# Kernel tuning notes

Measured on AMD Instinct MI355X. Metric: run time of the kernel, lower is better.

The kernel has to match this reference:

```python
import jax, jax.numpy as jnp
import numpy as np

N = 50000
E = 1600000
VOCAB = 1000
EMB = 128
HID = 128
OUT = 128


def setup_inputs() -> dict:
    key = jax.random.key(0)
    ks = jax.random.split(key, 8)
    labels = jax.random.randint(ks[0], (N,), 0, VOCAB)
    edge_index = jax.random.randint(ks[1], (2, E), 0, N)
    weight = jax.random.uniform(ks[2], (E,), dtype=jnp.float32)
    emb_table = jax.random.normal(ks[3], (VOCAB, EMB), dtype=jnp.float32) * 0.02
    W1 = jax.random.normal(ks[4], (EMB, HID), dtype=jnp.float32) * (1.0 / np.sqrt(EMB))
    b1 = jnp.zeros((HID,), dtype=jnp.float32)
    W2 = jax.random.normal(ks[5], (HID, OUT), dtype=jnp.float32) * (1.0 / np.sqrt(HID))
    b2 = jnp.zeros((OUT,), dtype=jnp.float32)
    return {"labels": labels, "edge_index": edge_index, "weight": weight,
            "emb_table": emb_table, "W1": W1, "b1": b1, "W2": W2, "b2": b2}


def _gcn_conv(x, src, dst, ew, W, b, n_nodes):
    # PyG GCNConv: linear transform, then symmetric-normalized weighted aggregation.
    x = x @ W  # [N, F_out]
    deg = jax.ops.segment_sum(ew, dst, num_segments=n_nodes)  # weighted in-degree (incl. self loops)
    dinv = jnp.where(deg > 0, jax.lax.rsqrt(deg), 0.0)
    norm = dinv[src] * ew * dinv[dst]  # [E_tot]
    msg = x[src] * norm[:, None]  # gather + scale
    out = jax.ops.segment_sum(msg, dst, num_segments=n_nodes)  # scatter-add
    return out + b


def reference(labels, edge_index, weight, emb_table, W1, b1, W2, b2):
    n_nodes = emb_table.shape[0] if False else labels.shape[0]
    # add self loops with weight 1.0 (GCNConv default add_self_loops=True)
    loop = jnp.arange(n_nodes, dtype=edge_index.dtype)
    src = jnp.concatenate([edge_index[0], loop])
    dst = jnp.concatenate([edge_index[1], loop])
    ew = jnp.concatenate([weight.astype(jnp.float32), jnp.ones((n_nodes,), jnp.float32)])

    x = emb_table[labels]  # embedding lookup [N, EMB]
    x = _gcn_conv(x, src, dst, ew, W1, b1, n_nodes)
    x = jax.nn.relu(x)
    x = _gcn_conv(x, src, dst, ew, W2, b2, n_nodes)
    return x
```

## Files before the change

kernel.cpp:

```cpp
#include <hip/hip_runtime.h>
#include <hip/hip_fp16.h>


#define CHUNKS 256

__global__ __launch_bounds__(256) void hist_kernel(const int* __restrict__ dst,
                                                   int* __restrict__ hist,
                                                   int e, int chunk, int nb) {
  __shared__ unsigned lh[1024];
  int b = blockIdx.x, t = threadIdx.x;
  int start = b * chunk, end = min(e, start + chunk);
  for (int i = t; i < nb; i += 256) lh[i] = 0;
  __syncthreads();
  for (int i = start + t; i < end; i += 256) atomicAdd(&lh[dst[i] >> 6], 1u);
  __syncthreads();
  for (int k = t; k < nb; k += 256) hist[(size_t)k * CHUNKS + b] = (int)lh[k];
}

__global__ __launch_bounds__(256) void colscan_kernel(const int* __restrict__ hist,
                                                      int* __restrict__ off,
                                                      int* __restrict__ tot,
                                                      int nb, int bact) {
  int k = (blockIdx.x * 256 + threadIdx.x) >> 6;
  int lane = threadIdx.x & 63;
  if (k >= nb) return;
  int carry = 0;
  for (int r = 0; r < CHUNKS / 64; ++r) {
    int b = r * 64 + lane;
    int h = (b < bact) ? hist[(size_t)k * CHUNKS + b] : 0;
    int x = h;
#pragma unroll
    for (int d = 1; d < 64; d <<= 1) {
      int tt = __shfl_up(x, d, 64);
      if (lane >= d) x += tt;
    }
    if (b < bact) off[(size_t)k * CHUNKS + b] = carry + x - h;
    carry += __shfl(x, 63, 64);
  }
  if (lane == 0) tot[k] = carry;
}

__global__ __launch_bounds__(1024) void ebase_kernel(const int* __restrict__ tot,
                                                     int* __restrict__ ebase, int nb) {
  __shared__ int wsum[16];
  int t = threadIdx.x, lane = t & 63, wv = t >> 6;
  int v = (t < nb) ? tot[t] : 0;
  int x = v;
#pragma unroll
  for (int d = 1; d < 64; d <<= 1) {
    int tt = __shfl_up(x, d, 64);
    if (lane >= d) x += tt;
  }
  if (lane == 63) wsum[wv] = x;
  __syncthreads();
  int o = 0;
#pragma unroll
  for (int w = 0; w < 16; ++w) o += (w < wv) ? wsum[w] : 0;
  int excl = x - v + o;
  if (t < nb) ebase[t] = excl;
  if (t == nb - 1) ebase[nb] = excl + v;
}

__global__ __launch_bounds__(256) void scatter_kernel(
    const int* __restrict__ src, const int* __restrict__ dst,
    const float* __restrict__ w, const int* __restrict__ labels,
    const int* __restrict__ off, const int* __restrict__ ebase,
    int2* __restrict__ brec, int e, int chunk) {
  __shared__ unsigned bincnt[1024];
  int b = blockIdx.x, t = threadIdx.x;
  int start = b * chunk, end = min(e, start + chunk);
  for (int i = t; i < 1024; i += 256) bincnt[i] = 0;
  __syncthreads();
  for (int bs0 = start; bs0 < end; bs0 += 1792) {
    int bend = min(end, bs0 + 1792);
    int s[7], d[7], lb[7], ps[7];
    float wv[7];
#pragma unroll
    for (int u = 0; u < 7; ++u) {
      int i = bs0 + u * 256 + t;
      bool ok = i < bend;
      s[u] = ok ? src[i] : 0;
      d[u] = ok ? dst[i] : 0;
      wv[u] = ok ? w[i] : 0.f;
    }
#pragma unroll
    for (int u = 0; u < 7; ++u) lb[u] = labels[s[u]];
#pragma unroll
    for (int u = 0; u < 7; ++u) {
      int k = d[u] >> 6;
      ps[u] = ebase[k] + off[(size_t)k * CHUNKS + b];
    }
#pragma unroll
    for (int u = 0; u < 7; ++u) {
      int i = bs0 + u * 256 + t;
      if (i < bend) {
        int k = d[u] >> 6;
        unsigned lr = atomicAdd(&bincnt[k], 1u);
        unsigned rx = (unsigned)s[u] | ((unsigned)(d[u] & 63) << 16) |
                      ((unsigned)lb[u] << 22);
        brec[ps[u] + (int)lr] = make_int2((int)rx, __float_as_int(wv[u]));
      }
    }
  }
}

__global__ __launch_bounds__(256) void bsort_kernel(const int2* __restrict__ brec,
                                                    const int* __restrict__ ebase,
                                                    int2* __restrict__ csr,
                                                    int* __restrict__ rs,
                                                    float* __restrict__ dinv, int n) {
  __shared__ unsigned h64[64];
  __shared__ unsigned cur[64];
  __shared__ float rsum[64];
  int k = blockIdx.x, t = threadIdx.x;
  int e0 = ebase[k], e1 = ebase[k + 1];
  if (t < 64) { h64[t] = 0; rsum[t] = 0.f; }
  __syncthreads();
  for (int i = e0 + t; i < e1; i += 256) {
    int2 r = brec[i];
    unsigned dl = ((unsigned)r.x >> 16) & 63u;
    atomicAdd(&h64[dl], 1u);
    atomicAdd(&rsum[dl], __int_as_float(r.y));
  }
  __syncthreads();
  if (t < 64) {
    int hv = (int)h64[t];
    int x = hv;
#pragma unroll
    for (int d = 1; d < 64; d <<= 1) {
      int tt = __shfl_up(x, d, 64);
      if (t >= d) x += tt;
    }
    int ex = x - hv;
    cur[t] = (unsigned)(e0 + ex);
    int v = k * 64 + t;
    if (v <= n) rs[v] = e0 + ex;
    if (v < n) dinv[v] = rsqrtf(1.0f + rsum[t]);
  }
  __syncthreads();
  for (int i = e0 + t; i < e1; i += 256) {
    int2 r = brec[i];
    unsigned rx = (unsigned)r.x;
    int dl = (int)((rx >> 16) & 63u);
    int pos = (int)atomicAdd(&cur[dl], 1u);
    csr[pos] = make_int2((int)((rx & 0xffffu) | ((rx >> 22) << 16)), r.y);
  }
}

__global__ void temb_kernel(const float* __restrict__ emb, const float* __restrict__ W1,
                            __half* __restrict__ temb) {
  int r = blockIdx.x, j = threadIdx.x;
  __shared__ float xs[128];
  xs[j] = emb[r * 128 + j];
  __syncthreads();
  float acc = 0.f;
#pragma unroll 8
  for (int k = 0; k < 128; ++k) acc = fmaf(xs[k], W1[k * 128 + j], acc);
  temb[r * 128 + j] = __float2half_rn(acc);
}

__device__ __forceinline__ void unpack4(float2 raw, float2& a, float2& b) {
  union { float f; __half2 h; } u0, u1;
  u0.f = raw.x;
  u1.f = raw.y;
  a = __half22float2(u0.h);
  b = __half22float2(u1.h);
}

__global__ __launch_bounds__(256) void agg1_kernel(
    const int* __restrict__ rs, const int2* __restrict__ csr,
    const float* __restrict__ dinv, const int* __restrict__ labels,
    const __half* __restrict__ temb, const float* __restrict__ b1,
    __half* __restrict__ out1, int n) {
  int wid = (blockIdx.x * blockDim.x + threadIdx.x) >> 6;
  int lane = threadIdx.x & 63;
  if (wid >= n) return;
  int half = lane >> 5, fl = lane & 31;
  float di = dinv[wid];
  float acc0, acc1, acc2, acc3;
  {
    int selfrow = labels[wid];
    float2 raw = ((const float2*)(temb + (size_t)selfrow * 128))[fl];
    float2 a, b;
    unpack4(raw, a, b);
    float ss = half ? 0.f : di;
    acc0 = a.x * ss; acc1 = a.y * ss; acc2 = b.x * ss; acc3 = b.y * ss;
  }
  int r1v = rs[wid + 1];
  for (int base = rs[wid]; base < r1v; base += 64) {
    int s = 0;
    float v = 0.f;
    if (base + lane < r1v) {
      int2 c = csr[base + lane];
      s = c.x;
      v = __int_as_float(c.y) * dinv[c.x & 0xffff];
    }
    int nb = min(64, r1v - base);
    int j = 0;
    for (; j + 16 <= nb; j += 16) {
#pragma unroll
      for (int u = 0; u < 8; ++u) {
        int jj = j + 2 * u + half;
        int sj = __shfl(s, jj, 64);
        float vj = __shfl(v, jj, 64);
        float2 raw = ((const float2*)(temb + (size_t)(sj >> 16) * 128))[fl];
        float2 a, b;
        unpack4(raw, a, b);
        acc0 = fmaf(a.x, vj, acc0); acc1 = fmaf(a.y, vj, acc1);
        acc2 = fmaf(b.x, vj, acc2); acc3 = fmaf(b.y, vj, acc3);
      }
    }
    for (; j + 2 <= nb; j += 2) {
      int jj = j + half;
      int sj = __shfl(s, jj, 64);
      float vj = __shfl(v, jj, 64);
      float2 raw = ((const float2*)(temb + (size_t)(sj >> 16) * 128))[fl];
      float2 a, b;
      unpack4(raw, a, b);
      acc0 = fmaf(a.x, vj, acc0); acc1 = fmaf(a.y, vj, acc1);
      acc2 = fmaf(b.x, vj, acc2); acc3 = fmaf(b.y, vj, acc3);
    }
    if (j < nb) {
      int sj = __shfl(s, j, 64);
      float vj0 = __shfl(v, j, 64);
      float vj = half ? 0.f : vj0;
      float2 raw = ((const float2*)(temb + (size_t)(sj >> 16) * 128))[fl];
      float2 a, b;
      unpack4(raw, a, b);
      acc0 = fmaf(a.x, vj, acc0); acc1 = fmaf(a.y, vj, acc1);
      acc2 = fmaf(b.x, vj, acc2); acc3 = fmaf(b.y, vj, acc3);
    }
  }
  acc0 += __shfl_xor(acc0, 32, 64);
  acc1 += __shfl_xor(acc1, 32, 64);
  acc2 += __shfl_xor(acc2, 32, 64);
  acc3 += __shfl_xor(acc3, 32, 64);
  if (half == 0) {
    float4 b4 = ((const float4*)b1)[fl];
    acc0 = fmaxf(fmaf(acc0, di, b4.x), 0.f);
    acc1 = fmaxf(fmaf(acc1, di, b4.y), 0.f);
    acc2 = fmaxf(fmaf(acc2, di, b4.z), 0.f);
    acc3 = fmaxf(fmaf(acc3, di, b4.w), 0.f);
    union { float2 f2; __half2 h2[2]; } o;
    o.h2[0] = __float22half2_rn(make_float2(acc0, acc1));
    o.h2[1] = __float22half2_rn(make_float2(acc2, acc3));
    ((float2*)(out1 + (size_t)wid * 128))[fl] = o.f2;
  }
}

__global__ __launch_bounds__(256) void agg2_kernel(
    const int* __restrict__ rs, const int2* __restrict__ csr,
    const float* __restrict__ dinv, const __half* __restrict__ h,
    float* __restrict__ out, int n) {
  int wid = (blockIdx.x * blockDim.x + threadIdx.x) >> 6;
  int lane = threadIdx.x & 63;
  if (wid >= n) return;
  int half = lane >> 5, fl = lane & 31;
  float di = dinv[wid];
  float acc0, acc1, acc2, acc3;
  {
    float2 raw = ((const float2*)(h + (size_t)wid * 128))[fl];
    float2 a, b;
    unpack4(raw, a, b);
    float ss = half ? 0.f : di;
    acc0 = a.x * ss; acc1 = a.y * ss; acc2 = b.x * ss; acc3 = b.y * ss;
  }
  int r1v = rs[wid + 1];
  for (int base = rs[wid]; base < r1v; base += 64) {
    int s = 0;
    float v = 0.f;
    if (base + lane < r1v) {
      int2 c = csr[base + lane];
      s = c.x;
      v = __int_as_float(c.y) * dinv[c.x & 0xffff];
    }
    int nb = min(64, r1v - base);
    int j = 0;
    for (; j + 16 <= nb; j += 16) {
#pragma unroll
      for (int u = 0; u < 8; ++u) {
        int jj = j + 2 * u + half;
        int sj = __shfl(s, jj, 64);
        float vj = __shfl(v, jj, 64);
        float2 raw = ((const float2*)(h + (size_t)(sj & 0xffff) * 128))[fl];
        float2 a, b;
        unpack4(raw, a, b);
        acc0 = fmaf(a.x, vj, acc0); acc1 = fmaf(a.y, vj, acc1);
        acc2 = fmaf(b.x, vj, acc2); acc3 = fmaf(b.y, vj, acc3);
      }
    }
    for (; j + 2 <= nb; j += 2) {
      int jj = j + half;
      int sj = __shfl(s, jj, 64);
      float vj = __shfl(v, jj, 64);
      float2 raw = ((const float2*)(h + (size_t)(sj & 0xffff) * 128))[fl];
      float2 a, b;
      unpack4(raw, a, b);
      acc0 = fmaf(a.x, vj, acc0); acc1 = fmaf(a.y, vj, acc1);
      acc2 = fmaf(b.x, vj, acc2); acc3 = fmaf(b.y, vj, acc3);
    }
    if (j < nb) {
      int sj = __shfl(s, j, 64);
      float vj0 = __shfl(v, j, 64);
      float vj = half ? 0.f : vj0;
      float2 raw = ((const float2*)(h + (size_t)(sj & 0xffff) * 128))[fl];
      float2 a, b;
      unpack4(raw, a, b);
      acc0 = fmaf(a.x, vj, acc0); acc1 = fmaf(a.y, vj, acc1);
      acc2 = fmaf(b.x, vj, acc2); acc3 = fmaf(b.y, vj, acc3);
    }
  }
  acc0 += __shfl_xor(acc0, 32, 64);
  acc1 += __shfl_xor(acc1, 32, 64);
  acc2 += __shfl_xor(acc2, 32, 64);
  acc3 += __shfl_xor(acc3, 32, 64);
  if (half == 0) {
    ((float4*)(out + (size_t)wid * 128))[fl] =
        make_float4(acc0 * di, acc1 * di, acc2 * di, acc3 * di);
  }
}

__global__ __launch_bounds__(256) void gemm_bias_kernel(float* __restrict__ y,
                                                        const float* __restrict__ W,
                                                        const float* __restrict__ bias,
                                                        int n) {
  __shared__ float xs[32][128];
  int tid = threadIdx.x;
  int tc = tid & 31;
  int tr = tid >> 5;
  int rb = blockIdx.x * 32;
  {
    const float4* xg = (const float4*)(y + (size_t)rb * 128);
    float4* xls = (float4*)&xs[0][0];
#pragma unroll
    for (int i = 0; i < 4; ++i) {
      int idx = tid + i * 256;
      int row = rb + (idx >> 5);
      float4 val = (row < n) ? xg[idx] : make_float4(0.f, 0.f, 0.f, 0.f);
      xls[idx] = val;
    }
  }
  __syncthreads();
  int j0 = tc * 4;
  float4 b4 = *(const float4*)(bias + j0);
  float acc[4][4];
#pragma unroll
  for (int r = 0; r < 4; ++r) {
    acc[r][0] = b4.x; acc[r][1] = b4.y; acc[r][2] = b4.z; acc[r][3] = b4.w;
  }
#pragma unroll 4
  for (int k = 0; k < 128; ++k) {
    float4 w4 = *(const float4*)(W + k * 128 + j0);
#pragma unroll
    for (int r = 0; r < 4; ++r) {
      float xv = xs[tr * 4 + r][k];
      acc[r][0] = fmaf(xv, w4.x, acc[r][0]);
      acc[r][1] = fmaf(xv, w4.y, acc[r][1]);
      acc[r][2] = fmaf(xv, w4.z, acc[r][2]);
      acc[r][3] = fmaf(xv, w4.w, acc[r][3]);
    }
  }
#pragma unroll
  for (int r = 0; r < 4; ++r) {
    int row = rb + tr * 4 + r;
    if (row < n)
      *(float4*)(y + (size_t)row * 128 + j0) =
          make_float4(acc[r][0], acc[r][1], acc[r][2], acc[r][3]);
  }
}

extern "C" void kernel_launch(void* const* d_in, const int* in_sizes, int n_in,
                              void* d_out, int out_size, void* d_ws, size_t ws_size,
                              hipStream_t stream) {
  const int* labels = (const int*)d_in[0];
  const int* edge_index = (const int*)d_in[1];
  const float* weight = (const float*)d_in[2];
  const float* emb = (const float*)d_in[3];
  const float* W1 = (const float*)d_in[4];
  const float* b1 = (const float*)d_in[5];
  const float* W2 = (const float*)d_in[6];
  const float* b2 = (const float*)d_in[7];

  int n = in_sizes[0];
  int e = in_sizes[1] / 2;
  int vocab = in_sizes[3] / 128;
  const int* srcp = edge_index;
  const int* dstp = edge_index + e;

  int nb = (n + 63) >> 6;
  int chunk = (e + CHUNKS - 1) / CHUNKS;
  int bact = (e + chunk - 1) / chunk;

  float* ws = (float*)d_ws;
  size_t o = 0;
  auto alloc_f = [&](size_t c) { float* p = ws + o; o += (c + 255) & ~(size_t)255; return p; };
  int*    hist  = (int*)alloc_f((size_t)nb * CHUNKS);
  int*    off   = (int*)alloc_f((size_t)nb * CHUNKS);
  int*    tot   = (int*)alloc_f(nb);
  int*    ebase = (int*)alloc_f(nb + 1);
  int2*   brec  = (int2*)alloc_f((size_t)e * 2);
  int*    rs    = (int*)alloc_f(n + 1);
  int2*   csr   = (int2*)alloc_f((size_t)e * 2);
  float*  dinv  = alloc_f(n);
  __half* temb  = (__half*)alloc_f((size_t)vocab * 64);
  __half* out1  = (__half*)alloc_f((size_t)n * 64);
  (void)ws_size;

  dim3 b256(256);
  int gagg = (int)(((size_t)n * 64 + 255) / 256);

  hist_kernel<<<bact, b256, 0, stream>>>(dstp, hist, e, chunk, nb);
  colscan_kernel<<<(nb * 64 + 255) / 256, b256, 0, stream>>>(hist, off, tot, nb, bact);
  ebase_kernel<<<1, 1024, 0, stream>>>(tot, ebase, nb);
  scatter_kernel<<<bact, b256, 0, stream>>>(srcp, dstp, weight, labels, off, ebase,
                                            brec, e, chunk);
  bsort_kernel<<<nb, b256, 0, stream>>>(brec, ebase, csr, rs, dinv, n);
  temb_kernel<<<vocab, 128, 0, stream>>>(emb, W1, temb);
  agg1_kernel<<<gagg, b256, 0, stream>>>(rs, csr, dinv, labels, temb, b1, out1, n);
  agg2_kernel<<<gagg, b256, 0, stream>>>(rs, csr, dinv, out1, (float*)d_out, n);
  gemm_bias_kernel<<<(n + 31) / 32, b256, 0, stream>>>((float*)d_out, W2, b2, n);
}
```

Baseline: 200.5 us.

## Column-chunk layer-2 features and aggregate in four L2-resident passes

```diff
diff --git a/kernel.cpp b/kernel.cpp
--- a/kernel.cpp
+++ b/kernel.cpp
@@ -171,7 +171,7 @@
     const int* __restrict__ rs, const int2* __restrict__ csr,
     const float* __restrict__ dinv, const int* __restrict__ labels,
     const __half* __restrict__ temb, const float* __restrict__ b1,
-    __half* __restrict__ out1, int n) {
+    __half* __restrict__ out1c, int n) {
   int wid = (blockIdx.x * blockDim.x + threadIdx.x) >> 6;
   int lane = threadIdx.x & 63;
   if (wid >= n) return;
@@ -244,78 +244,58 @@
     union { float2 f2; __half2 h2[2]; } o;
     o.h2[0] = __float22half2_rn(make_float2(acc0, acc1));
     o.h2[1] = __float22half2_rn(make_float2(acc2, acc3));
-    ((float2*)(out1 + (size_t)wid * 128))[fl] = o.f2;
-  }
-}
-
-__global__ __launch_bounds__(256) void agg2_kernel(
+    ((float2*)(out1c + (((size_t)(fl >> 3) * n + wid) * 32)))[fl & 7] = o.f2;
+  }
+}
+
+__global__ __launch_bounds__(256) void agg2c_kernel(
     const int* __restrict__ rs, const int2* __restrict__ csr,
-    const float* __restrict__ dinv, const __half* __restrict__ h,
-    float* __restrict__ out, int n) {
+    const float* __restrict__ dinv, const __half* __restrict__ hc,
+    float* __restrict__ out, int n, int c) {
   int wid = (blockIdx.x * blockDim.x + threadIdx.x) >> 6;
   int lane = threadIdx.x & 63;
   if (wid >= n) return;
-  int half = lane >> 5, fl = lane & 31;
+  int grp = lane >> 3, fl = lane & 7;
   float di = dinv[wid];
-  float acc0, acc1, acc2, acc3;
-  {
-    float2 raw = ((const float2*)(h + (size_t)wid * 128))[fl];
+  float acc0 = 0.f, acc1 = 0.f, acc2 = 0.f, acc3 = 0.f;
+  if (grp == 0) {
+    float2 raw = ((const float2*)(hc + (size_t)wid * 32))[fl];
     float2 a, b;
     unpack4(raw, a, b);
-    float ss = half ? 0.f : di;
-    acc0 = a.x * ss; acc1 = a.y * ss; acc2 = b.x * ss; acc3 = b.y * ss;
+    acc0 = a.x * di; acc1 = a.y * di; acc2 = b.x * di; acc3 = b.y * di;
   }
   int r1v = rs[wid + 1];
   for (int base = rs[wid]; base < r1v; base += 64) {
     int s = 0;
     float v = 0.f;
     if (base + lane < r1v) {
-      int2 c = csr[base + lane];
-      s = c.x;
-      v = __int_as_float(c.y) * dinv[c.x & 0xffff];
+      int2 cc = csr[base + lane];
+      s = cc.x;
+      v = __int_as_float(cc.y) * dinv[cc.x & 0xffff];
     }
     int nb = min(64, r1v - base);
-    int j = 0;
-    for (; j + 16 <= nb; j += 16) {
-#pragma unroll
-      for (int u = 0; u < 8; ++u) {
-        int jj = j + 2 * u + half;
-        int sj = __shfl(s, jj, 64);
-        float vj = __shfl(v, jj, 64);
-        float2 raw = ((const float2*)(h + (size_t)(sj & 0xffff) * 128))[fl];
+#pragma unroll
+    for (int jstep = 0; jstep < 8; ++jstep) {
+      if (jstep * 8 < nb) {
+        int j = jstep * 8 + grp;
+        int sj = __shfl(s, j, 64);
+        float vj = __shfl(v, j, 64);
+        float2 raw = ((const float2*)(hc + (size_t)(sj & 0xffff) * 32))[fl];
         float2 a, b;
         unpack4(raw, a, b);
         acc0 = fmaf(a.x, vj, acc0); acc1 = fmaf(a.y, vj, acc1);
         acc2 = fmaf(b.x, vj, acc2); acc3 = fmaf(b.y, vj, acc3);
       }
     }
-    for (; j + 2 <= nb; j += 2) {
-      int jj = j + half;
-      int sj = __shfl(s, jj, 64);
-      float vj = __shfl(v, jj, 64);
-      float2 raw = ((const float2*)(h + (size_t)(sj & 0xffff) * 128))[fl];
-      float2 a, b;
-      unpack4(raw, a, b);
-      acc0 = fmaf(a.x, vj, acc0); acc1 = fmaf(a.y, vj, acc1);
-      acc2 = fmaf(b.x, vj, acc2); acc3 = fmaf(b.y, vj, acc3);
-    }
-    if (j < nb) {
-      int sj = __shfl(s, j, 64);
-      float vj0 = __shfl(v, j, 64);
-      float vj = half ? 0.f : vj0;
-      float2 raw = ((const float2*)(h + (size_t)(sj & 0xffff) * 128))[fl];
-      float2 a, b;
-      unpack4(raw, a, b);
-      acc0 = fmaf(a.x, vj, acc0); acc1 = fmaf(a.y, vj, acc1);
-      acc2 = fmaf(b.x, vj, acc2); acc3 = fmaf(b.y, vj, acc3);
-    }
-  }
-  acc0 += __shfl_xor(acc0, 32, 64);
-  acc1 += __shfl_xor(acc1, 32, 64);
-  acc2 += __shfl_xor(acc2, 32, 64);
-  acc3 += __shfl_xor(acc3, 32, 64);
-  if (half == 0) {
-    ((float4*)(out + (size_t)wid * 128))[fl] =
+  }
+  acc0 += __shfl_xor(acc0, 8, 64);  acc1 += __shfl_xor(acc1, 8, 64);
+  acc2 += __shfl_xor(acc2, 8, 64);  acc3 += __shfl_xor(acc3, 8, 64);
+  acc0 += __shfl_xor(acc0, 16, 64); acc1 += __shfl_xor(acc1, 16, 64);
+  acc2 += __shfl_xor(acc2, 16, 64); acc3 += __shfl_xor(acc3, 16, 64);
+  acc0 += __shfl_xor(acc0, 32, 64); acc1 += __shfl_xor(acc1, 32, 64);
+  acc2 += __shfl_xor(acc2, 32, 64); acc3 += __shfl_xor(acc3, 32, 64);
+  if (grp == 0) {
+    ((float4*)(out + (size_t)wid * 128 + 32 * c))[fl] =
         make_float4(acc0 * di, acc1 * di, acc2 * di, acc3 * di);
   }
 }
@@ -403,7 +383,7 @@
   int2*   csr   = (int2*)alloc_f((size_t)e * 2);
   float*  dinv  = alloc_f(n);
   __half* temb  = (__half*)alloc_f((size_t)vocab * 64);
-  __half* out1  = (__half*)alloc_f((size_t)n * 64);
+  __half* out1c = (__half*)alloc_f((size_t)n * 64);
   (void)ws_size;
 
   dim3 b256(256);
@@ -416,7 +396,11 @@
                                             brec, e, chunk);
   bsort_kernel<<<nb, b256, 0, stream>>>(brec, ebase, csr, rs, dinv, n);
   temb_kernel<<<vocab, 128, 0, stream>>>(emb, W1, temb);
-  agg1_kernel<<<gagg, b256, 0, stream>>>(rs, csr, dinv, labels, temb, b1, out1, n);
-  agg2_kernel<<<gagg, b256, 0, stream>>>(rs, csr, dinv, out1, (float*)d_out, n);
+  agg1_kernel<<<gagg, b256, 0, stream>>>(rs, csr, dinv, labels, temb, b1, out1c, n);
+  for (int c = 0; c < 4; ++c) {
+    agg2c_kernel<<<gagg, b256, 0, stream>>>(rs, csr, dinv,
+                                            out1c + (size_t)c * n * 32,
+                                            (float*)d_out, n, c);
+  }
   gemm_bias_kernel<<<(n + 31) / 32, b256, 0, stream>>>((float*)d_out, W2, b2, n);
 }
```

Result: slower. 259.8 us (+29.6%).

## Widen sort-phase blocks to 1024 threads, cache bin bases, stage bucket records in LDS

Applied to the files above, without the earlier changes.

```diff
diff --git a/kernel.cpp b/kernel.cpp
--- a/kernel.cpp
+++ b/kernel.cpp
@@ -3,18 +3,19 @@
 
 
 #define CHUNKS 256
-
-__global__ __launch_bounds__(256) void hist_kernel(const int* __restrict__ dst,
-                                                   int* __restrict__ hist,
-                                                   int e, int chunk, int nb) {
+#define BSTAGE 2816
+
+__global__ __launch_bounds__(1024) void hist_kernel(const int* __restrict__ dst,
+                                                    int* __restrict__ hist,
+                                                    int e, int chunk, int nb) {
   __shared__ unsigned lh[1024];
   int b = blockIdx.x, t = threadIdx.x;
+  lh[t] = 0;
+  __syncthreads();
   int start = b * chunk, end = min(e, start + chunk);
-  for (int i = t; i < nb; i += 256) lh[i] = 0;
-  __syncthreads();
-  for (int i = start + t; i < end; i += 256) atomicAdd(&lh[dst[i] >> 6], 1u);
-  __syncthreads();
-  for (int k = t; k < nb; k += 256) hist[(size_t)k * CHUNKS + b] = (int)lh[k];
+  for (int i = start + t; i < end; i += 1024) atomicAdd(&lh[dst[i] >> 6], 1u);
+  __syncthreads();
+  if (t < nb) hist[(size_t)t * CHUNKS + b] = (int)lh[t];
 }
 
 __global__ __launch_bounds__(256) void colscan_kernel(const int* __restrict__ hist,
@@ -61,45 +62,41 @@
   if (t == nb - 1) ebase[nb] = excl + v;
 }
 
-__global__ __launch_bounds__(256) void scatter_kernel(
+__global__ __launch_bounds__(1024) void scatter_kernel(
     const int* __restrict__ src, const int* __restrict__ dst,
     const float* __restrict__ w, const int* __restrict__ labels,
     const int* __restrict__ off, const int* __restrict__ ebase,
-    int2* __restrict__ brec, int e, int chunk) {
+    int2* __restrict__ brec, int e, int chunk, int nb) {
   __shared__ unsigned bincnt[1024];
+  __shared__ int gbase[1024];
   int b = blockIdx.x, t = threadIdx.x;
+  bincnt[t] = 0;
+  if (t < nb) gbase[t] = ebase[t] + off[(size_t)t * CHUNKS + b];
+  __syncthreads();
   int start = b * chunk, end = min(e, start + chunk);
-  for (int i = t; i < 1024; i += 256) bincnt[i] = 0;
-  __syncthreads();
-  for (int bs0 = start; bs0 < end; bs0 += 1792) {
-    int bend = min(end, bs0 + 1792);
-    int s[7], d[7], lb[7], ps[7];
-    float wv[7];
-#pragma unroll
-    for (int u = 0; u < 7; ++u) {
-      int i = bs0 + u * 256 + t;
-      bool ok = i < bend;
-      s[u] = ok ? src[i] : 0;
-      d[u] = ok ? dst[i] : 0;
-      wv[u] = ok ? w[i] : 0.f;
-    }
-#pragma unroll
-    for (int u = 0; u < 7; ++u) lb[u] = labels[s[u]];
-#pragma unroll
-    for (int u = 0; u < 7; ++u) {
+  int s[7], d[7], lb[7], ps[7];
+  float wv[7];
+#pragma unroll
+  for (int u = 0; u < 7; ++u) {
+    int i = start + u * 1024 + t;
+    bool ok = i < end;
+    s[u] = ok ? src[i] : 0;
+    d[u] = ok ? dst[i] : 0;
+    wv[u] = ok ? w[i] : 0.f;
+  }
+#pragma unroll
+  for (int u = 0; u < 7; ++u) lb[u] = labels[s[u]];
+#pragma unroll
+  for (int u = 0; u < 7; ++u) ps[u] = gbase[d[u] >> 6];
+#pragma unroll
+  for (int u = 0; u < 7; ++u) {
+    int i = start + u * 1024 + t;
+    if (i < end) {
       int k = d[u] >> 6;
-      ps[u] = ebase[k] + off[(size_t)k * CHUNKS + b];
-    }
-#pragma unroll
-    for (int u = 0; u < 7; ++u) {
-      int i = bs0 + u * 256 + t;
-      if (i < bend) {
-        int k = d[u] >> 6;
-        unsigned lr = atomicAdd(&bincnt[k], 1u);
-        unsigned rx = (unsigned)s[u] | ((unsigned)(d[u] & 63) << 16) |
-                      ((unsigned)lb[u] << 22);
-        brec[ps[u] + (int)lr] = make_int2((int)rx, __float_as_int(wv[u]));
-      }
+      unsigned lr = atomicAdd(&bincnt[k], 1u);
+      unsigned rx = (unsigned)s[u] | ((unsigned)(d[u] & 63) << 16) |
+                    ((unsigned)lb[u] << 22);
+      brec[ps[u] + (int)lr] = make_int2((int)rx, __float_as_int(wv[u]));
     }
   }
 }
@@ -109,15 +106,18 @@
                                                     int2* __restrict__ csr,
                                                     int* __restrict__ rs,
                                                     float* __restrict__ dinv, int n) {
+  __shared__ int2 stage[BSTAGE];
   __shared__ unsigned h64[64];
   __shared__ unsigned cur[64];
   __shared__ float rsum[64];
   int k = blockIdx.x, t = threadIdx.x;
-  int e0 = ebase[k], e1 = ebase[k + 1];
+  int e0 = ebase[k], e1 = ebase[k + 1], cnt = e1 - e0;
   if (t < 64) { h64[t] = 0; rsum[t] = 0.f; }
   __syncthreads();
-  for (int i = e0 + t; i < e1; i += 256) {
-    int2 r = brec[i];
+  bool fits = (cnt <= BSTAGE);
+  for (int i = t; i < cnt; i += 256) {
+    int2 r = brec[e0 + i];
+    if (fits) stage[i] = r;
     unsigned dl = ((unsigned)r.x >> 16) & 63u;
     atomicAdd(&h64[dl], 1u);
     atomicAdd(&rsum[dl], __int_as_float(r.y));
@@ -138,8 +138,8 @@
     if (v < n) dinv[v] = rsqrtf(1.0f + rsum[t]);
   }
   __syncthreads();
-  for (int i = e0 + t; i < e1; i += 256) {
-    int2 r = brec[i];
+  for (int i = t; i < cnt; i += 256) {
+    int2 r = fits ? stage[i] : brec[e0 + i];
     unsigned rx = (unsigned)r.x;
     int dl = (int)((rx >> 16) & 63u);
     int pos = (int)atomicAdd(&cur[dl], 1u);
@@ -407,13 +407,14 @@
   (void)ws_size;
 
   dim3 b256(256);
+  dim3 b1024(1024);
   int gagg = (int)(((size_t)n * 64 + 255) / 256);
 
-  hist_kernel<<<bact, b256, 0, stream>>>(dstp, hist, e, chunk, nb);
+  hist_kernel<<<bact, b1024, 0, stream>>>(dstp, hist, e, chunk, nb);
   colscan_kernel<<<(nb * 64 + 255) / 256, b256, 0, stream>>>(hist, off, tot, nb, bact);
-  ebase_kernel<<<1, 1024, 0, stream>>>(tot, ebase, nb);
-  scatter_kernel<<<bact, b256, 0, stream>>>(srcp, dstp, weight, labels, off, ebase,
-                                            brec, e, chunk);
+  ebase_kernel<<<1, b1024, 0, stream>>>(tot, ebase, nb);
+  scatter_kernel<<<bact, b1024, 0, stream>>>(srcp, dstp, weight, labels, off, ebase,
+                                             brec, e, chunk, nb);
   bsort_kernel<<<nb, b256, 0, stream>>>(brec, ebase, csr, rs, dinv, n);
   temb_kernel<<<vocab, 128, 0, stream>>>(emb, W1, temb);
   agg1_kernel<<<gagg, b256, 0, stream>>>(rs, csr, dinv, labels, temb, b1, out1, n);
```

Result: faster. 186.1 us (-7.2%).
